# Kernel tuning notes

Hardware: AMD Instinct MI355X
Metric: run time of the kernel (lower is better)

The kernel has to match this reference:

```python
import jax, jax.numpy as jnp
import numpy as np

B, T, C = 8, 4096, 768


def wkv(w, u, k, v):
    """RWKV WKV linear recurrence with running max/exp state.
    w, u: (C,) ; k, v: (B, T, C) -> y: (B, T, C), all float32.
    Faithful to wkv_pytorch: note w is ADDED to pp (no negation/exp).
    """
    kt = jnp.swapaxes(k, 0, 1)  # (T, B, C)
    vt = jnp.swapaxes(v, 0, 1)

    def step(carry, inp):
        aa, bb, pp = carry            # each (B, C)
        k_t, v_t = inp                # each (B, C)
        ww = u[None, :] + k_t
        p = jnp.maximum(pp, ww)
        e1 = jnp.exp(pp - p)
        e2 = jnp.exp(ww - p)
        y_t = (e1 * aa + e2 * v_t) / (e1 * bb + e2)
        ww2 = w[None, :] + pp
        p2 = jnp.maximum(ww2, k_t)
        e1b = jnp.exp(ww2 - p2)
        e2b = jnp.exp(k_t - p2)
        aa = e1b * aa + e2b * v_t
        bb = e1b * bb + e2b
        return (aa, bb, p2), y_t

    init = (jnp.zeros((B, C), jnp.float32),
            jnp.zeros((B, C), jnp.float32),
            jnp.full((B, C), -1e38, jnp.float32))
    _, y = jax.lax.scan(step, init, (kt, vt))
    return jnp.swapaxes(y, 0, 1)  # (B, T, C)


def setup_inputs() -> dict:
    key = jax.random.key(0)
    ks = jax.random.split(key, 7)
    scale = 1.0 / np.sqrt(C)
    x = jax.random.normal(ks[0], (B, T, C), jnp.float32)
    w_key = jax.random.normal(ks[1], (C, C), jnp.float32) * scale
    w_value = jax.random.normal(ks[2], (C, C), jnp.float32) * scale
    w_receptance = jax.random.normal(ks[3], (C, C), jnp.float32) * scale
    w_output = jax.random.normal(ks[4], (C, C), jnp.float32) * scale
    # 'fancy' init, layer_id=5, n_layer=12
    layer_id, n_layer = 5, 12
    ratio_0_to_1 = layer_id / (n_layer - 1)
    h = np.arange(C, dtype=np.float64)
    spatial_decay = (-5.0 + 8.0 * (h / (C - 1)) ** (0.7 + 1.3 * ratio_0_to_1)).astype(np.float32)
    zigzag = (np.array([(i + 1) % 3 - 1 for i in range(C)], dtype=np.float64) * 0.5)
    spatial_first = (np.ones(C) * np.log(0.3) + zigzag).astype(np.float32)
    return {
        "x": x,
        "w_key": w_key,
        "w_value": w_value,
        "w_receptance": w_receptance,
        "w_output": w_output,
        "spatial_decay": jnp.asarray(spatial_decay),
        "spatial_first": jnp.asarray(spatial_first),
    }


def reference(x, w_key, w_value, w_receptance, w_output, spatial_decay, spatial_first):
    # shift_pixel=0, empty spatial_shift_list -> xk = xv = xr = x
    k = jnp.einsum('btc,oc->bto', x, w_key)
    v = jnp.einsum('btc,oc->bto', x, w_value)
    sr = jax.nn.sigmoid(jnp.einsum('btc,oc->bto', x, w_receptance))
    y = wkv(spatial_decay / T, spatial_first / T, k, v)
    out = jnp.einsum('btc,oc->bto', sr * y, w_output)
    return out
```

## Files before the change

### kernel.cpp

```cpp
#include <hip/hip_runtime.h>
#include <hip/hip_bf16.h>

using bf16 = __hip_bfloat16;
typedef short bf16x8v  __attribute__((ext_vector_type(8)));
typedef float f32x16v  __attribute__((ext_vector_type(16)));

#define GLD_LDS16(g, l) __builtin_amdgcn_global_load_lds(                      \
    (const __attribute__((address_space(1))) void*)(g),                        \
    (__attribute__((address_space(3))) void*)(l), 16, 0, 0)

__device__ __forceinline__ float bflo(unsigned int u) {
  union { unsigned int i; float f; } c; c.i = u << 16; return c.f;
}
__device__ __forceinline__ float bfhi(unsigned int u) {
  union { unsigned int i; float f; } c; c.i = u & 0xffff0000u; return c.f;
}
__device__ __forceinline__ unsigned int packbf(float a, float b) {
  return (unsigned int)(__hip_bfloat16_raw(__float2bfloat16(a)).x) |
         ((unsigned int)(__hip_bfloat16_raw(__float2bfloat16(b)).x) << 16);
}
__device__ __forceinline__ unsigned short bfraw(float a) {
  return __hip_bfloat16_raw(__float2bfloat16(a)).x;
}

__global__ void f2b4_all(const float* __restrict__ x,  const float* __restrict__ wk,
                         const float* __restrict__ wv, const float* __restrict__ wr,
                         const float* __restrict__ wo,
                         bf16* __restrict__ x_bf, bf16* __restrict__ wcat,
                         bf16* __restrict__ wo_bf) {
  int i = blockIdx.x * blockDim.x + threadIdx.x;
  const float* s; bf16* d; int idx;
  if (i < 6291456) { s = x; d = x_bf; idx = i; }
  else {
    int j = i - 6291456;
    int seg = j / 147456;
    idx = j - seg * 147456;
    if (seg == 0)      { s = wk; d = wcat; }
    else if (seg == 1) { s = wv; d = wcat + 589824; }
    else if (seg == 2) { s = wr; d = wcat + 1179648; }
    else               { s = wo; d = wo_bf; }
  }
  const float4 f = reinterpret_cast<const float4*>(s)[idx];
  struct B4 { bf16 a, b, c, d; };
  B4 o = { __float2bfloat16(f.x), __float2bfloat16(f.y),
           __float2bfloat16(f.z), __float2bfloat16(f.w) };
  reinterpret_cast<B4*>(d)[idx] = o;
}

__device__ __forceinline__ void gemm_tile_acc(
    const bf16* __restrict__ A, const bf16* __restrict__ W,
    bf16* lds_a, bf16* lds_b, int tid, size_t m0, int n0, f32x16v acc[2])
{
  const int lane = tid & 63;
  const int wave = tid >> 6;
  const int l31  = lane & 31;
  const int hi   = lane >> 5;
  const int wr   = (wave >> 2) * 64;
  const int wc   = (wave & 3) * 32;

  int srow[2], scol[2];
#pragma unroll
  for (int q = 0; q < 2; ++q) {
    const int s = tid + q * 512;
    srow[q] = s >> 3;
    scol[q] = (((s & 7) ^ (srow[q] & 7)) * 8);
  }

#pragma unroll
  for (int i = 0; i < 2; ++i)
#pragma unroll
    for (int r = 0; r < 16; ++r) acc[i][r] = 0.0f;

  for (int k0 = 0; k0 < 768; k0 += 64) {
    __syncthreads();
#pragma unroll
    for (int q = 0; q < 2; ++q)
      GLD_LDS16(A + (m0 + srow[q]) * 768 + k0 + scol[q], &lds_a[(size_t)(tid + q * 512) * 8]);
#pragma unroll
    for (int q = 0; q < 2; ++q)
      GLD_LDS16(W + (size_t)(n0 + srow[q]) * 768 + k0 + scol[q], &lds_b[(size_t)(tid + q * 512) * 8]);
    __syncthreads();

#pragma unroll
    for (int ks = 0; ks < 4; ++ks) {
      const int gl = ks * 2 + hi;
      bf16x8v av[2], bv;
#pragma unroll
      for (int i = 0; i < 2; ++i) {
        const int ra = wr + 32 * i + l31;
        av[i] = *(const bf16x8v*)&lds_a[ra * 64 + ((gl ^ (ra & 7)) * 8)];
      }
      {
        const int rb = wc + l31;
        bv = *(const bf16x8v*)&lds_b[rb * 64 + ((gl ^ (rb & 7)) * 8)];
      }
#pragma unroll
      for (int i = 0; i < 2; ++i)
        acc[i] = __builtin_amdgcn_mfma_f32_32x32x16_bf16(bv, av[i], acc[i], 0, 0, 0);
    }
  }
}


__global__ __launch_bounds__(512) void gemm_kvr(
    const bf16* __restrict__ A, const bf16* __restrict__ Wcat,
    bf16* __restrict__ Kb, bf16* __restrict__ Vb, bf16* __restrict__ SRb)
{
  __shared__ __align__(16) bf16 lds_a[128 * 64];
  __shared__ __align__(16) bf16 lds_b[128 * 64];
  const int tid = threadIdx.x;
  const int bx = blockIdx.x;
  const int chunk = bx / 1152;
  const int rem   = bx % 1152;
  const int mm    = rem & 63;
  const int nt    = rem >> 6;
  const size_t m0 = (size_t)(chunk * 64 + mm) * 128;
  const int n0 = nt * 128;

  f32x16v acc[2];
  gemm_tile_acc(A, Wcat, lds_a, lds_b, tid, m0, n0, acc);

  const int seg   = n0 / 768;
  const int ncol0 = n0 - seg * 768;
  bf16* __restrict__ dst = (seg == 0) ? Kb : (seg == 1) ? Vb : SRb;
  const int lane = tid & 63, wave = tid >> 6;
  const int l31 = lane & 31, hi = lane >> 5;
  const int wr = (wave >> 2) * 64, wc = (wave & 3) * 32;
#pragma unroll
  for (int i = 0; i < 2; ++i) {
    const size_t mrow = m0 + wr + 32 * i + l31;
    const int nb = ncol0 + wc + 4 * hi;
#pragma unroll
    for (int rr = 0; rr < 4; ++rr) {
      float v0 = acc[i][4 * rr + 0], v1 = acc[i][4 * rr + 1];
      float v2 = acc[i][4 * rr + 2], v3 = acc[i][4 * rr + 3];
      if (seg == 2) {
        v0 = 1.0f / (1.0f + __expf(-v0)); v1 = 1.0f / (1.0f + __expf(-v1));
        v2 = 1.0f / (1.0f + __expf(-v2)); v3 = 1.0f / (1.0f + __expf(-v3));
      }
      ushort4 pk = { bfraw(v0), bfraw(v1), bfraw(v2), bfraw(v3) };
      *(ushort4*)&dst[mrow * 768 + nb + 8 * rr] = pk;
    }
  }
}

__global__ __launch_bounds__(512) void gemm_out(
    const bf16* __restrict__ A, const bf16* __restrict__ W,
    float* __restrict__ out)
{
  __shared__ __align__(16) bf16 lds_a[128 * 64];
  __shared__ __align__(16) bf16 lds_b[128 * 64];
  const int tid = threadIdx.x;
  const int bx = blockIdx.x;
  const int chunk = bx / 384;
  const int rem   = bx % 384;
  const int mm    = rem & 63;
  const int nt    = rem >> 6;
  const size_t m0 = (size_t)(chunk * 64 + mm) * 128;
  const int n0 = nt * 128;

  f32x16v acc[2];
  gemm_tile_acc(A, W, lds_a, lds_b, tid, m0, n0, acc);

  const int lane = tid & 63, wave = tid >> 6;
  const int l31 = lane & 31, hi = lane >> 5;
  const int wr = (wave >> 2) * 64, wc = (wave & 3) * 32;
#pragma unroll
  for (int i = 0; i < 2; ++i) {
    const size_t mrow = m0 + wr + 32 * i + l31;
    const int nb = n0 + wc + 4 * hi;
#pragma unroll
    for (int rr = 0; rr < 4; ++rr) {
      float4 pk = { acc[i][4 * rr + 0], acc[i][4 * rr + 1],
                    acc[i][4 * rr + 2], acc[i][4 * rr + 3] };
      *(float4*)&out[mrow * 768 + nb + 8 * rr] = pk;
    }
  }
}

__global__ void wkv_phaseA(const bf16* __restrict__ K, const bf16* __restrict__ V,
                           const float* __restrict__ sd,
                           float* __restrict__ sA, float* __restrict__ sB, float* __restrict__ sP)
{
  const int idx = blockIdx.x * 256 + threadIdx.x;
  const int c4 = idx % 192;
  const int bg = idx / 192;
  const int g  = bg & 127;
  const int b  = bg >> 7;
  const int c0 = c4 * 4;
  float w[4], aa[4], bb[4], pp[4];
#pragma unroll
  for (int e = 0; e < 4; ++e) {
    w[e] = sd[c0 + e] * (1.0f / 4096.0f);
    aa[e] = 0.f; bb[e] = 0.f; pp[e] = -1e38f;
  }
  const size_t base = ((size_t)b * 4096 + (size_t)g * 32) * 768 + c0;
  const uint2* Kp = (const uint2*)(K + base);
  const uint2* Vp = (const uint2*)(V + base);
#pragma unroll 4
  for (int t = 0; t < 32; ++t) {
    const uint2 ku = Kp[(size_t)t * 192];
    const uint2 vu = Vp[(size_t)t * 192];
    const float kc[4] = { bflo(ku.x), bfhi(ku.x), bflo(ku.y), bfhi(ku.y) };
    const float vc[4] = { bflo(vu.x), bfhi(vu.x), bflo(vu.y), bfhi(vu.y) };
#pragma unroll
    for (int e = 0; e < 4; ++e) {
      const float ww2 = w[e] + pp[e];
      const float p2  = fmaxf(ww2, kc[e]);
      const float e1b = __expf(ww2 - p2);
      const float e2b = __expf(kc[e] - p2);
      aa[e] = e1b * aa[e] + e2b * vc[e];
      bb[e] = e1b * bb[e] + e2b;
      pp[e] = p2;
    }
  }
  const int o = g * 6144 + b * 768 + c0;
#pragma unroll
  for (int e = 0; e < 4; ++e) { sA[o + e] = aa[e]; sB[o + e] = bb[e]; sP[o + e] = pp[e]; }
}

__global__ void wkv_phaseB(const float* __restrict__ sA, const float* __restrict__ sB,
                           const float* __restrict__ sP,
                           float* __restrict__ iA, float* __restrict__ iB, float* __restrict__ iP,
                           const float* __restrict__ sd)
{
  const int bc = blockIdx.x;
  const int g  = threadIdx.x;
  const int c  = bc % 768;
  const float Lw = 32.0f * (sd[c] * (1.0f / 4096.0f));
  __shared__ float sa[128], sb[128], sp[128], sl[128];
  const int o = g * 6144 + bc;
  float a = sA[o], b = sB[o], p = sP[o], L = Lw;
  sa[g] = a; sb[g] = b; sp[g] = p; sl[g] = L;
  __syncthreads();
#pragma unroll
  for (int d = 1; d < 128; d <<= 1) {
    float a2 = a, b2 = b, p2 = p, L2 = L;
    if (g >= d) {
      const float al = sa[g - d], bl = sb[g - d], pl = sp[g - d], Ll = sl[g - d];
      const float pn = fmaxf(pl + L, p);
      const float e0 = __expf(pl + L - pn);
      const float e1 = __expf(p - pn);
      a2 = e0 * al + e1 * a;
      b2 = e0 * bl + e1 * b;
      p2 = pn;
      L2 = Ll + L;
    }
    __syncthreads();
    sa[g] = a2; sb[g] = b2; sp[g] = p2; sl[g] = L2;
    a = a2; b = b2; p = p2; L = L2;
    __syncthreads();
  }
  float oa = 0.f, ob = 0.f, op = -1e38f;
  if (g > 0) { oa = sa[g - 1]; ob = sb[g - 1]; op = sp[g - 1]; }
  iA[o] = oa; iB[o] = ob; iP[o] = op;
}

__global__ void wkv_phaseC(const bf16* __restrict__ K, const bf16* __restrict__ V,
                           const bf16* __restrict__ SR,
                           const float* __restrict__ iA, const float* __restrict__ iB,
                           const float* __restrict__ iP,
                           const float* __restrict__ sd, const float* __restrict__ sf,
                           bf16* __restrict__ RY)
{
  const int idx = blockIdx.x * 256 + threadIdx.x;
  const int c4 = idx % 192;
  const int bg = idx / 192;
  const int g  = bg & 127;
  const int b  = bg >> 7;
  const int c0 = c4 * 4;
  const int o = g * 6144 + b * 768 + c0;
  float w[4], u[4], aa[4], bb[4], pp[4];
#pragma unroll
  for (int e = 0; e < 4; ++e) {
    w[e] = sd[c0 + e] * (1.0f / 4096.0f);
    u[e] = sf[c0 + e] * (1.0f / 4096.0f);
    aa[e] = iA[o + e]; bb[e] = iB[o + e]; pp[e] = iP[o + e];
  }
  const size_t base = ((size_t)b * 4096 + (size_t)g * 32) * 768 + c0;
  const uint2* Kp = (const uint2*)(K + base);
  const uint2* Vp = (const uint2*)(V + base);
  const uint2* Sp = (const uint2*)(SR + base);
  uint2* Rp = (uint2*)(RY + base);
#pragma unroll 4
  for (int t = 0; t < 32; ++t) {
    const uint2 ku = Kp[(size_t)t * 192];
    const uint2 vu = Vp[(size_t)t * 192];
    const uint2 su = Sp[(size_t)t * 192];
    const float kc[4] = { bflo(ku.x), bfhi(ku.x), bflo(ku.y), bfhi(ku.y) };
    const float vc[4] = { bflo(vu.x), bfhi(vu.x), bflo(vu.y), bfhi(vu.y) };
    const float sc[4] = { bflo(su.x), bfhi(su.x), bflo(su.y), bfhi(su.y) };
    float y[4];
#pragma unroll
    for (int e = 0; e < 4; ++e) {
      const float ww = u[e] + kc[e];
      const float p  = fmaxf(pp[e], ww);
      const float e1 = __expf(pp[e] - p);
      const float e2 = __expf(ww - p);
      y[e] = (e1 * aa[e] + e2 * vc[e]) / (e1 * bb[e] + e2) * sc[e];
      const float ww2 = w[e] + pp[e];
      const float p2  = fmaxf(ww2, kc[e]);
      const float e1b = __expf(ww2 - p2);
      const float e2b = __expf(kc[e] - p2);
      aa[e] = e1b * aa[e] + e2b * vc[e];
      bb[e] = e1b * bb[e] + e2b;
      pp[e] = p2;
    }
    uint2 r; r.x = packbf(y[0], y[1]); r.y = packbf(y[2], y[3]);
    Rp[(size_t)t * 192] = r;
  }
}

extern "C" void kernel_launch(void* const* d_in, const int* in_sizes, int n_in,
                              void* d_out, int out_size, void* d_ws, size_t ws_size,
                              hipStream_t stream)
{
  const float* x  = (const float*)d_in[0];
  const float* wk = (const float*)d_in[1];
  const float* wv = (const float*)d_in[2];
  const float* wr = (const float*)d_in[3];
  const float* wo = (const float*)d_in[4];
  const float* sd = (const float*)d_in[5];
  const float* sf = (const float*)d_in[6];
  float* out = (float*)d_out;

  char* ws = (char*)d_ws;
  bf16*  x_bf  = (bf16*) (ws + 0);
  bf16*  wcat  = (bf16*) (ws + 50331648);
  bf16*  wo_bf = (bf16*) (ws + 53870592);
  bf16*  Kb    = (bf16*) (ws + 55050240);
  bf16*  Vb    = (bf16*) (ws + 105381888);
  bf16*  SRb   = (bf16*) (ws + 155713536);
  float* sumA  = (float*)(ws + 206045184);
  float* sumB  = (float*)(ws + 209190912);
  float* sumP  = (float*)(ws + 212336640);
  float* iniA  = (float*)(ws + 215482368);
  float* iniB  = (float*)(ws + 218628096);
  float* iniP  = (float*)(ws + 221773824);
  bf16*  ry_bf = x_bf;

  f2b4_all<<<26880, 256, 0, stream>>>(x, wk, wv, wr, wo, x_bf, wcat, wo_bf);

  gemm_kvr<<<4608, 512, 0, stream>>>(x_bf, wcat, Kb, Vb, SRb);

  wkv_phaseA<<<768, 256, 0, stream>>>(Kb, Vb, sd, sumA, sumB, sumP);
  wkv_phaseB<<<6144, 128, 0, stream>>>(sumA, sumB, sumP, iniA, iniB, iniP, sd);
  wkv_phaseC<<<768, 256, 0, stream>>>(Kb, Vb, SRb, iniA, iniB, iniP, sd, sf, ry_bf);

  gemm_out<<<1536, 512, 0, stream>>>(ry_bf, wo_bf, out);
}
```

Baseline: 498.2 us.

## Double-buffer GEMM LDS tiles and replace phaseB tree scan with sequential scan

The shared GEMM mainloop now uses two LDS buffers, issuing the async global-to-LDS load for the next K slice before computing on the current one, so memory latency can overlap MFMA work. This halves the barriers per slice but doubles LDS per block to 64 KB, which may reduce occupancy. Separately, the chunk-combine phaseB drops its 128-thread log-step Hillis-Steele scan (6144 blocks, many barriers) for 96 blocks that stage 64 channels into LDS. One wave then runs a serial 128-step exclusive scan per channel. That wave does far less total work but runs long dependent chains on very few CUs.

```diff
diff --git a/kernel.cpp b/kernel.cpp
--- a/kernel.cpp
+++ b/kernel.cpp
@@ -47,10 +47,52 @@
   reinterpret_cast<B4*>(d)[idx] = o;
 }
 
+__device__ __forceinline__ void stg64(
+    const bf16* __restrict__ A, const bf16* __restrict__ W,
+    bf16* la, bf16* lb, int k0, size_t m0, int n0,
+    const int srow[2], const int scol[2], int tid)
+{
+#pragma unroll
+  for (int q = 0; q < 2; ++q) {
+    GLD_LDS16(A + (m0 + srow[q]) * 768 + k0 + scol[q],
+              &la[(size_t)(tid + q * 512) * 8]);
+    GLD_LDS16(W + ((size_t)n0 + srow[q]) * 768 + k0 + scol[q],
+              &lb[(size_t)(tid + q * 512) * 8]);
+  }
+}
+
+__device__ __forceinline__ void comp64(
+    const bf16* la, const bf16* lb, int wr, int wc, int l31, int hi,
+    f32x16v acc[2])
+{
+#pragma unroll
+  for (int ks = 0; ks < 4; ++ks) {
+    const int gl = ks * 2 + hi;
+    bf16x8v av[2], bv;
+#pragma unroll
+    for (int i = 0; i < 2; ++i) {
+      const int ra = wr + 32 * i + l31;
+      av[i] = *(const bf16x8v*)&la[ra * 64 + ((gl ^ (ra & 7)) * 8)];
+    }
+    {
+      const int rb = wc + l31;
+      bv = *(const bf16x8v*)&lb[rb * 64 + ((gl ^ (rb & 7)) * 8)];
+    }
+#pragma unroll
+    for (int i = 0; i < 2; ++i)
+      acc[i] = __builtin_amdgcn_mfma_f32_32x32x16_bf16(bv, av[i], acc[i], 0, 0, 0);
+  }
+}
+
 __device__ __forceinline__ void gemm_tile_acc(
     const bf16* __restrict__ A, const bf16* __restrict__ W,
-    bf16* lds_a, bf16* lds_b, int tid, size_t m0, int n0, f32x16v acc[2])
-{
+    bf16* lds, int tid, size_t m0, int n0, f32x16v acc[2])
+{
+  bf16* const a0 = lds;
+  bf16* const b0 = lds + 8192;
+  bf16* const a1 = lds + 16384;
+  bf16* const b1 = lds + 24576;
+
   const int lane = tid & 63;
   const int wave = tid >> 6;
   const int l31  = lane & 31;
@@ -71,33 +113,15 @@
 #pragma unroll
     for (int r = 0; r < 16; ++r) acc[i][r] = 0.0f;
 
-  for (int k0 = 0; k0 < 768; k0 += 64) {
+  stg64(A, W, a0, b0, 0, m0, n0, srow, scol, tid);
+
+  for (int t = 0; t < 12; t += 2) {
     __syncthreads();
-#pragma unroll
-    for (int q = 0; q < 2; ++q)
-      GLD_LDS16(A + (m0 + srow[q]) * 768 + k0 + scol[q], &lds_a[(size_t)(tid + q * 512) * 8]);
-#pragma unroll
-    for (int q = 0; q < 2; ++q)
-      GLD_LDS16(W + (size_t)(n0 + srow[q]) * 768 + k0 + scol[q], &lds_b[(size_t)(tid + q * 512) * 8]);
+    if (t + 1 < 12) stg64(A, W, a1, b1, (t + 1) * 64, m0, n0, srow, scol, tid);
+    comp64(a0, b0, wr, wc, l31, hi, acc);
     __syncthreads();
-
-#pragma unroll
-    for (int ks = 0; ks < 4; ++ks) {
-      const int gl = ks * 2 + hi;
-      bf16x8v av[2], bv;
-#pragma unroll
-      for (int i = 0; i < 2; ++i) {
-        const int ra = wr + 32 * i + l31;
-        av[i] = *(const bf16x8v*)&lds_a[ra * 64 + ((gl ^ (ra & 7)) * 8)];
-      }
-      {
-        const int rb = wc + l31;
-        bv = *(const bf16x8v*)&lds_b[rb * 64 + ((gl ^ (rb & 7)) * 8)];
-      }
-#pragma unroll
-      for (int i = 0; i < 2; ++i)
-        acc[i] = __builtin_amdgcn_mfma_f32_32x32x16_bf16(bv, av[i], acc[i], 0, 0, 0);
-    }
+    if (t + 2 < 12) stg64(A, W, a0, b0, (t + 2) * 64, m0, n0, srow, scol, tid);
+    comp64(a1, b1, wr, wc, l31, hi, acc);
   }
 }
 
@@ -106,8 +130,7 @@
     const bf16* __restrict__ A, const bf16* __restrict__ Wcat,
     bf16* __restrict__ Kb, bf16* __restrict__ Vb, bf16* __restrict__ SRb)
 {
-  __shared__ __align__(16) bf16 lds_a[128 * 64];
-  __shared__ __align__(16) bf16 lds_b[128 * 64];
+  __shared__ __align__(16) bf16 lds[32768];
   const int tid = threadIdx.x;
   const int bx = blockIdx.x;
   const int chunk = bx / 1152;
@@ -118,7 +141,7 @@
   const int n0 = nt * 128;
 
   f32x16v acc[2];
-  gemm_tile_acc(A, Wcat, lds_a, lds_b, tid, m0, n0, acc);
+  gemm_tile_acc(A, Wcat, lds, tid, m0, n0, acc);
 
   const int seg   = n0 / 768;
   const int ncol0 = n0 - seg * 768;
@@ -148,8 +171,7 @@
     const bf16* __restrict__ A, const bf16* __restrict__ W,
     float* __restrict__ out)
 {
-  __shared__ __align__(16) bf16 lds_a[128 * 64];
-  __shared__ __align__(16) bf16 lds_b[128 * 64];
+  __shared__ __align__(16) bf16 lds[32768];
   const int tid = threadIdx.x;
   const int bx = blockIdx.x;
   const int chunk = bx / 384;
@@ -160,7 +182,7 @@
   const int n0 = nt * 128;
 
   f32x16v acc[2];
-  gemm_tile_acc(A, W, lds_a, lds_b, tid, m0, n0, acc);
+  gemm_tile_acc(A, W, lds, tid, m0, n0, acc);
 
   const int lane = tid & 63, wave = tid >> 6;
   const int l31 = lane & 31, hi = lane >> 5;
@@ -219,41 +241,40 @@
   for (int e = 0; e < 4; ++e) { sA[o + e] = aa[e]; sB[o + e] = bb[e]; sP[o + e] = pp[e]; }
 }
 
-__global__ void wkv_phaseB(const float* __restrict__ sA, const float* __restrict__ sB,
-                           const float* __restrict__ sP,
-                           float* __restrict__ iA, float* __restrict__ iB, float* __restrict__ iP,
-                           const float* __restrict__ sd)
-{
-  const int bc = blockIdx.x;
-  const int g  = threadIdx.x;
-  const int c  = bc % 768;
-  const float Lw = 32.0f * (sd[c] * (1.0f / 4096.0f));
-  __shared__ float sa[128], sb[128], sp[128], sl[128];
-  const int o = g * 6144 + bc;
-  float a = sA[o], b = sB[o], p = sP[o], L = Lw;
-  sa[g] = a; sb[g] = b; sp[g] = p; sl[g] = L;
+__global__ __launch_bounds__(256) void wkv_phaseB(
+    const float* __restrict__ sA, const float* __restrict__ sB,
+    const float* __restrict__ sP,
+    float* __restrict__ iA, float* __restrict__ iB, float* __restrict__ iP,
+    const float* __restrict__ sd)
+{
+  __shared__ float la[128][64], lb[128][64], lp[128][64];
+  const int bc0 = blockIdx.x * 64;
+  const int tid = threadIdx.x;
+  const int gr = tid >> 6;
+  const int cc = tid & 63;
+  for (int g0 = 0; g0 < 128; g0 += 4) {
+    const int g = g0 + gr;
+    const int o = g * 6144 + bc0 + cc;
+    la[g][cc] = sA[o]; lb[g][cc] = sB[o]; lp[g][cc] = sP[o];
+  }
   __syncthreads();
-#pragma unroll
-  for (int d = 1; d < 128; d <<= 1) {
-    float a2 = a, b2 = b, p2 = p, L2 = L;
-    if (g >= d) {
-      const float al = sa[g - d], bl = sb[g - d], pl = sp[g - d], Ll = sl[g - d];
-      const float pn = fmaxf(pl + L, p);
-      const float e0 = __expf(pl + L - pn);
-      const float e1 = __expf(p - pn);
-      a2 = e0 * al + e1 * a;
-      b2 = e0 * bl + e1 * b;
-      p2 = pn;
-      L2 = Ll + L;
-    }
-    __syncthreads();
-    sa[g] = a2; sb[g] = b2; sp[g] = p2; sl[g] = L2;
-    a = a2; b = b2; p = p2; L = L2;
-    __syncthreads();
-  }
-  float oa = 0.f, ob = 0.f, op = -1e38f;
-  if (g > 0) { oa = sa[g - 1]; ob = sb[g - 1]; op = sp[g - 1]; }
-  iA[o] = oa; iB[o] = ob; iP[o] = op;
+  if (tid < 64) {
+    const int c = bc0 + tid;
+    const float Lw = 32.0f * (sd[c % 768] * (1.0f / 4096.0f));
+    float aa = 0.f, bb = 0.f, pp = -1e38f;
+    for (int g = 0; g < 128; ++g) {
+      const int o = g * 6144 + c;
+      iA[o] = aa; iB[o] = bb; iP[o] = pp;
+      const float lag = la[g][tid], lbg = lb[g][tid], lpg = lp[g][tid];
+      const float pd = pp + Lw;
+      const float pn = fmaxf(pd, lpg);
+      const float e0 = __expf(pd - pn);
+      const float e1 = __expf(lpg - pn);
+      aa = e0 * aa + e1 * lag;
+      bb = e0 * bb + e1 * lbg;
+      pp = pn;
+    }
+  }
 }
 
 __global__ void wkv_phaseC(const bf16* __restrict__ K, const bf16* __restrict__ V,
@@ -344,7 +365,7 @@
   gemm_kvr<<<4608, 512, 0, stream>>>(x_bf, wcat, Kb, Vb, SRb);
 
   wkv_phaseA<<<768, 256, 0, stream>>>(Kb, Vb, sd, sumA, sumB, sumP);
-  wkv_phaseB<<<6144, 128, 0, stream>>>(sumA, sumB, sumP, iniA, iniB, iniP, sd);
+  wkv_phaseB<<<96, 256, 0, stream>>>(sumA, sumB, sumP, iniA, iniB, iniP, sd);
   wkv_phaseC<<<768, 256, 0, stream>>>(Kb, Vb, SRb, iniA, iniB, iniP, sd, sf, ry_bf);
 
   gemm_out<<<1536, 512, 0, stream>>>(ry_bf, wo_bf, out);
```

Result: faster. 445.9 us (-10.5%).
